# Performance work log

Measured on AMD Instinct MI355X. Metric: run time of the kernel, lower is better.

Reference implementation:

```python
import jax, jax.numpy as jnp
import numpy as np

N_NODES = 100000
N_EDGES = 1600000
N_GRAPHS = 256
IN_F = 64   # global_features (GNN input dim)
OUT_F = 64  # node_features (GNN output dim)


def setup_inputs() -> dict:
    key = jax.random.key(0)
    ks = jax.random.split(key, 8)
    x = jax.random.normal(ks[0], (N_NODES, IN_F), dtype=jnp.float32)
    edge_index = jax.random.randint(ks[1], (2, N_EDGES), 0, N_NODES, dtype=jnp.int64)
    batch = jnp.sort(jax.random.randint(ks[2], (N_NODES,), 0, N_GRAPHS, dtype=jnp.int64))
    # GNNLayer linear: in=global_features, out=node_features
    W_gnn = jax.random.normal(ks[3], (IN_F, OUT_F), dtype=jnp.float32) / np.sqrt(IN_F)
    b_gnn = jnp.zeros((OUT_F,), dtype=jnp.float32)
    # global_attention: Linear(node_features, 1)
    W_att = jax.random.normal(ks[4], (OUT_F, 1), dtype=jnp.float32) / np.sqrt(OUT_F)
    b_att = jnp.zeros((1,), dtype=jnp.float32)
    return {"x": x, "edge_index": edge_index, "batch": batch,
            "W_gnn": W_gnn, "b_gnn": b_gnn, "W_att": W_att, "b_att": b_att}


def reference(x, edge_index, batch, W_gnn, b_gnn, W_att, b_att):
    src, dst = edge_index[0], edge_index[1]
    # --- GNN message passing layer: aggregate neighbor features, transform ---
    agg = jax.ops.segment_sum(x[src], dst, num_segments=N_NODES)  # [N, IN_F]
    h = jax.nn.relu((x + agg) @ W_gnn + b_gnn)                    # [N, OUT_F]
    # --- attention scores + scatter softmax over batch segments ---
    scores = (h @ W_att + b_att)[:, 0]                            # [N]
    seg_max = jax.ops.segment_max(scores, batch, num_segments=N_GRAPHS)
    e = jnp.exp(scores - seg_max[batch])
    denom = jax.ops.segment_sum(e, batch, num_segments=N_GRAPHS)
    w = e / denom[batch]                                          # [N]
    # --- weighted scatter-add pooling ---
    out = jax.ops.segment_sum(w[:, None] * h, batch, num_segments=N_GRAPHS)
    return out  # [N_GRAPHS, OUT_F]
```

## Files before the change

### kernel.cpp

```cpp
#include <hip/hip_runtime.h>

#define N_NODES  100000
#define N_EDGES  1600000
#define N_GRAPHS 256
#define F        64

#define CHUNK    8192
#define NCHUNK   196
#define GBN      128
#define NB2      782
#define EDGE_CAP 2560

#define CAST_ELEMS   (N_NODES * F / 4)
#define CAST_BLOCKS  ((CAST_ELEMS + 1023) / 1024)
#define PREP_BLOCKS  (NCHUNK + CAST_BLOCKS)

__device__ __forceinline__ unsigned short f2bf(float f) {
    unsigned int u = __float_as_uint(f);
    u += 0x7FFFu + ((u >> 16) & 1u);
    return (unsigned short)(u >> 16);
}

__global__ __launch_bounds__(1024) void prep_kernel(
        const float* __restrict__ x, unsigned short* __restrict__ xh,
        const int* __restrict__ src, const int* __restrict__ dst,
        unsigned int* __restrict__ pairs, int* __restrict__ cstartT,
        float* __restrict__ out, float* __restrict__ denom) {
    int tid = threadIdx.x;
    int b   = blockIdx.x;

    if (b >= NCHUNK) {
        int ci = b - NCHUNK;
        if (ci == 0) {
            for (int i = tid; i < N_GRAPHS * F; i += 1024) out[i] = 0.f;
            if (tid < N_GRAPHS) denom[tid] = 0.f;
        }
        int i = ci * 1024 + tid;
        if (i < CAST_ELEMS) {
            float4 v = ((const float4*)x)[i];
            ushort4 o;
            o.x = f2bf(v.x); o.y = f2bf(v.y); o.z = f2bf(v.z); o.w = f2bf(v.w);
            ((ushort4*)xh)[i] = o;
        }
        return;
    }

    __shared__ int hist[NB2];
    __shared__ int cur[NB2];
    __shared__ int wsum[16];
    __shared__ unsigned int stage[CHUNK];
    int c    = b;
    int base = c * CHUNK;
    int m    = min(CHUNK, N_EDGES - base);
    int lane = tid & 63;
    int w    = tid >> 6;

    for (int k = tid; k < NB2; k += 1024) hist[k] = 0;
    __syncthreads();
    for (int e = tid; e < m; e += 1024)
        atomicAdd(&hist[dst[base + e] >> 7], 1);
    __syncthreads();

    int v = (tid < NB2) ? hist[tid] : 0;
    #pragma unroll
    for (int o = 1; o < 64; o <<= 1) {
        int u = __shfl_up(v, o, 64);
        if (lane >= o) v += u;
    }
    if (lane == 63) wsum[w] = v;
    __syncthreads();
    if (tid < 16) {
        int s = wsum[tid];
        #pragma unroll
        for (int o = 1; o < 16; o <<= 1) {
            int u = __shfl_up(s, o, 64);
            if (tid >= o) s += u;
        }
        wsum[tid] = s;
    }
    __syncthreads();
    if (w > 0) v += wsum[w - 1];

    if (tid < NB2) {
        int excl = v - hist[tid];
        cur[tid] = excl;
        cstartT[tid * NCHUNK + c] = base + excl;
    }
    if (tid == 0) cstartT[NB2 * NCHUNK + c] = base + m;
    __syncthreads();
    for (int e = tid; e < m; e += 1024) {
        int d = dst[base + e];
        int slot = atomicAdd(&cur[d >> 7], 1);
        stage[slot] = ((unsigned)(d & (GBN - 1)) << 17) | (unsigned)src[base + e];
    }
    __syncthreads();
    for (int e = tid; e < m; e += 1024)
        pairs[base + e] = stage[e];
}

__global__ __launch_bounds__(512) void compact_kernel(
        const unsigned int* __restrict__ pairs,
        const int* __restrict__ cstartT,
        int* __restrict__ eidx,
        int* __restrict__ nbeg,
        int* __restrict__ nend) {
    __shared__ int rstart[NCHUNK];
    __shared__ int rcnt[NCHUNK];
    __shared__ int roff[NCHUNK];
    __shared__ int wsum[8];
    __shared__ int Etot_s;
    __shared__ unsigned int epairs[EDGE_CAP];
    __shared__ int ncnt[GBN];
    __shared__ int ncur[GBN];

    int tid   = threadIdx.x;
    int wave  = tid >> 6;
    int lane  = tid & 63;
    int b     = blockIdx.x;
    int node0 = b * GBN;
    int nn    = min(GBN, N_NODES - node0);
    int gbase = b * EDGE_CAP;

    int myrc = 0;
    if (tid < NCHUNK) {
        int a = cstartT[b * NCHUNK + tid];
        int n = cstartT[(b + 1) * NCHUNK + tid];
        rstart[tid] = a;
        rcnt[tid]   = n - a;
        myrc = n - a;
    }
    __syncthreads();

    {
        int v = myrc;
        #pragma unroll
        for (int o = 1; o < 64; o <<= 1) {
            int u = __shfl_up(v, o, 64);
            if (lane >= o) v += u;
        }
        if (lane == 63) wsum[wave] = v;
        __syncthreads();
        if (tid < 8) {
            int s = wsum[tid];
            #pragma unroll
            for (int o = 1; o < 8; o <<= 1) {
                int u = __shfl_up(s, o, 64);
                if (tid >= o) s += u;
            }
            wsum[tid] = s;
        }
        __syncthreads();
        if (wave > 0) v += wsum[wave - 1];
        if (tid < NCHUNK) roff[tid] = v - myrc;
        if (tid == NCHUNK - 1) Etot_s = v;
    }
    __syncthreads();
    int E = Etot_s;

    for (int r = wave; r < NCHUNK; r += 8) {
        int cr = rcnt[r];
        for (int l = lane; l < cr; l += 64)
            epairs[roff[r] + l] = pairs[rstart[r] + l];
    }
    __syncthreads();

    if (tid < GBN) ncnt[tid] = 0;
    __syncthreads();
    for (int e = tid; e < E; e += 512)
        atomicAdd(&ncnt[epairs[e] >> 17], 1);
    __syncthreads();
    {
        int mycnt = (tid < GBN) ? ncnt[tid] : 0;
        int v = mycnt;
        #pragma unroll
        for (int o = 1; o < 64; o <<= 1) {
            int u = __shfl_up(v, o, 64);
            if (lane >= o) v += u;
        }
        if (lane == 63) wsum[wave] = v;
        __syncthreads();
        if (tid < 8) {
            int s = wsum[tid];
            #pragma unroll
            for (int o = 1; o < 8; o <<= 1) {
                int u = __shfl_up(s, o, 64);
                if (tid >= o) s += u;
            }
            wsum[tid] = s;
        }
        __syncthreads();
        if (wave > 0) v += wsum[wave - 1];
        if (tid < GBN) {
            int excl = v - mycnt;
            ncur[tid] = excl;
            if (tid < nn) {
                nbeg[node0 + tid] = gbase + excl;
                nend[node0 + tid] = gbase + excl + mycnt;
            }
        }
    }
    __syncthreads();
    for (int e = tid; e < E; e += 512) {
        unsigned int p = epairs[e];
        int slot = atomicAdd(&ncur[p >> 17], 1);
        eidx[gbase + slot] = (int)(p & 0x1FFFFu);
    }
}

#define NODES_PER_WAVE 25
#define GT_NWAVES  (N_NODES / NODES_PER_WAVE)
#define GT_BLOCKS  (GT_NWAVES / 4)

__device__ __forceinline__ float bfl(unsigned int u) { return __uint_as_float(u << 16); }
__device__ __forceinline__ float bfh(unsigned int u) { return __uint_as_float(u & 0xFFFF0000u); }

__global__ __launch_bounds__(256) void gather_pool_kernel(
        const unsigned short* __restrict__ xh,
        const int*   __restrict__ nbeg,
        const int*   __restrict__ nend,
        const int*   __restrict__ eidx,
        const int*   __restrict__ batch,
        const float* __restrict__ Wg,
        const float* __restrict__ bg,
        const float* __restrict__ Wa,
        const float* __restrict__ ba,
        float*       __restrict__ out_acc,
        float*       __restrict__ denom) {
    int tid  = threadIdx.x;
    int lane = tid & 63;
    int grp  = lane >> 3;
    int c    = lane & 7;
    int waveId = blockIdx.x * 4 + (tid >> 6);

    int n0   = waveId * NODES_PER_WAVE;
    int nEnd = n0 + NODES_PER_WAVE;

    float wcol[F];
    #pragma unroll
    for (int k = 0; k < F; ++k) wcol[k] = Wg[k * F + lane];
    float bgl = bg[lane];
    float wal = Wa[lane];
    float ba0 = ba[0];

    const uint4* xh4 = (const uint4*)xh;

    int   cur_g = batch[n0];
    float accw  = 0.f;
    float denw  = 0.f;

    int pb = nbeg[n0];
    int pe = nend[n0];
    int sl_cur = (pb + lane < pe) ? eidx[pb + lane] : 0;

    for (int n = n0; n < nEnd; ++n) {
        int start = pb, end = pe;
        int sl    = sl_cur;
        if (n + 1 < nEnd) {
            pb = nbeg[n + 1];
            pe = nend[n + 1];
            sl_cur = (pb + lane < pe) ? eidx[pb + lane] : 0;
        }

        float a0=0.f,a1=0.f,a2=0.f,a3=0.f,a4=0.f,a5=0.f,a6=0.f,a7=0.f;
        {
            int jmax = end - start; if (jmax > 64) jmax = 64;
            for (int j = 0; j < jmax; j += 8) {
                int el = j + grp;
                int s  = __shfl(sl, el, 64);
                if (el < jmax) {
                    uint4 v = xh4[s * 8 + c];
                    a0 += bfl(v.x); a1 += bfh(v.x);
                    a2 += bfl(v.y); a3 += bfh(v.y);
                    a4 += bfl(v.z); a5 += bfh(v.z);
                    a6 += bfl(v.w); a7 += bfh(v.w);
                }
            }
        }
        for (int base = start + 64; base < end; base += 64) {
            int jmax = end - base; if (jmax > 64) jmax = 64;
            int sl2 = (base + lane < end) ? eidx[base + lane] : 0;
            for (int j = 0; j < jmax; j += 8) {
                int el = j + grp;
                int s  = __shfl(sl2, el, 64);
                if (el < jmax) {
                    uint4 v = xh4[s * 8 + c];
                    a0 += bfl(v.x); a1 += bfh(v.x);
                    a2 += bfl(v.y); a3 += bfh(v.y);
                    a4 += bfl(v.z); a5 += bfh(v.z);
                    a6 += bfl(v.w); a7 += bfh(v.w);
                }
            }
        }
        #pragma unroll
        for (int o = 8; o <= 32; o <<= 1) {
            a0 += __shfl_xor(a0, o, 64); a1 += __shfl_xor(a1, o, 64);
            a2 += __shfl_xor(a2, o, 64); a3 += __shfl_xor(a3, o, 64);
            a4 += __shfl_xor(a4, o, 64); a5 += __shfl_xor(a5, o, 64);
            a6 += __shfl_xor(a6, o, 64); a7 += __shfl_xor(a7, o, 64);
        }
        {
            uint4 v = xh4[n * 8 + c];
            a0 += bfl(v.x); a1 += bfh(v.x);
            a2 += bfl(v.y); a3 += bfh(v.y);
            a4 += bfl(v.z); a5 += bfh(v.z);
            a6 += bfl(v.w); a7 += bfh(v.w);
        }

        float re[8] = {a0,a1,a2,a3,a4,a5,a6,a7};
        float q0=0.f,q1=0.f,q2=0.f,q3=0.f,q4=0.f,q5=0.f,q6=0.f,q7=0.f;
        #pragma unroll
        for (int k = 0; k < F; k += 8) {
            int ln = k >> 3;
            q0 += __int_as_float(__builtin_amdgcn_readlane(__float_as_int(re[0]), ln)) * wcol[k + 0];
            q1 += __int_as_float(__builtin_amdgcn_readlane(__float_as_int(re[1]), ln)) * wcol[k + 1];
            q2 += __int_as_float(__builtin_amdgcn_readlane(__float_as_int(re[2]), ln)) * wcol[k + 2];
            q3 += __int_as_float(__builtin_amdgcn_readlane(__float_as_int(re[3]), ln)) * wcol[k + 3];
            q4 += __int_as_float(__builtin_amdgcn_readlane(__float_as_int(re[4]), ln)) * wcol[k + 4];
            q5 += __int_as_float(__builtin_amdgcn_readlane(__float_as_int(re[5]), ln)) * wcol[k + 5];
            q6 += __int_as_float(__builtin_amdgcn_readlane(__float_as_int(re[6]), ln)) * wcol[k + 6];
            q7 += __int_as_float(__builtin_amdgcn_readlane(__float_as_int(re[7]), ln)) * wcol[k + 7];
        }
        float hv = ((q0 + q1) + (q2 + q3)) + ((q4 + q5) + (q6 + q7)) + bgl;
        hv = hv > 0.f ? hv : 0.f;

        float p = hv * wal;
        #pragma unroll
        for (int o = 32; o > 0; o >>= 1)
            p += __shfl_down(p, o, 64);
        float s = __int_as_float(__builtin_amdgcn_readlane(__float_as_int(p), 0)) + ba0;
        float e = __expf(s);

        int g = batch[n];
        if (g != cur_g) {
            atomicAdd(&out_acc[cur_g * F + lane], accw);
            if (lane == 0) atomicAdd(&denom[cur_g], denw);
            accw = 0.f; denw = 0.f; cur_g = g;
        }
        accw += e * hv;
        denw += e;
    }
    atomicAdd(&out_acc[cur_g * F + lane], accw);
    if (lane == 0) atomicAdd(&denom[cur_g], denw);
}

__global__ __launch_bounds__(256) void finalize_kernel(
        float* __restrict__ out, const float* __restrict__ denom) {
    int i = blockIdx.x * 256 + threadIdx.x;
    if (i >= N_GRAPHS * F) return;
    float d = denom[i >> 6];
    out[i] = (d > 0.f) ? out[i] / d : 0.f;
}

extern "C" void kernel_launch(void* const* d_in, const int* in_sizes, int n_in,
                              void* d_out, int out_size, void* d_ws, size_t ws_size,
                              hipStream_t stream) {
    const float* x     = (const float*)d_in[0];
    const int*   ei    = (const int*)d_in[1];
    const int*   batch = (const int*)d_in[2];
    const float* Wg    = (const float*)d_in[3];
    const float* bg    = (const float*)d_in[4];
    const float* Wa    = (const float*)d_in[5];
    const float* ba    = (const float*)d_in[6];
    float* out = (float*)d_out;

    const int* src = ei;
    const int* dst = ei + N_EDGES;

    char* ws = (char*)d_ws;
    unsigned short* xh      = (unsigned short*)(ws);
    unsigned int*   pairs   = (unsigned int*)(ws + 12800000);
    int*            cstartT = (int*)(ws + 19200000);
    int*            eidx    = (int*)(ws + 19814144);
    int*            nbeg    = (int*)(ws + 27821824);
    int*            nend    = (int*)(ws + 28221824);
    float*          denom   = (float*)(ws + 28621824);

    prep_kernel       <<<PREP_BLOCKS, 1024, 0, stream>>>(
        x, xh, src, dst, pairs, cstartT, out, denom);
    compact_kernel    <<<NB2, 512, 0, stream>>>(pairs, cstartT, eidx, nbeg, nend);
    gather_pool_kernel<<<GT_BLOCKS, 256, 0, stream>>>(
        xh, nbeg, nend, eidx, batch, Wg, bg, Wa, ba, out, denom);
    finalize_kernel   <<<(N_GRAPHS * F + 255) / 256, 256, 0, stream>>>(out, denom);
}
```

Baseline: 189.4 us.

## Move x bf16 cast into compact kernel and flatten segment copy with binary search

The fp32-to-bf16 cast of x and the zeroing of the output now run as extra blocks of the compact kernel instead of the prep kernel, so the prep histogram blocks no longer share a launch with cast work. The compact kernel goes from 512 to 1024 threads. Its per-chunk copy, one wave per segment, is replaced by a flat per-element loop that finds each element's source segment with a binary search over the prefix offsets, which balances load across threads. The cost is extra search work per element and a larger block that may lower occupancy.

```diff
diff --git a/kernel.cpp b/kernel.cpp
--- a/kernel.cpp
+++ b/kernel.cpp
@@ -13,7 +13,7 @@
 
 #define CAST_ELEMS   (N_NODES * F / 4)
 #define CAST_BLOCKS  ((CAST_ELEMS + 1023) / 1024)
-#define PREP_BLOCKS  (NCHUNK + CAST_BLOCKS)
+#define CPF_BLOCKS   (NB2 + CAST_BLOCKS)
 
 __device__ __forceinline__ unsigned short f2bf(float f) {
     unsigned int u = __float_as_uint(f);
@@ -22,15 +22,76 @@
 }
 
 __global__ __launch_bounds__(1024) void prep_kernel(
-        const float* __restrict__ x, unsigned short* __restrict__ xh,
         const int* __restrict__ src, const int* __restrict__ dst,
-        unsigned int* __restrict__ pairs, int* __restrict__ cstartT,
+        unsigned int* __restrict__ pairs, int* __restrict__ cstartT) {
+    __shared__ int hist[NB2];
+    __shared__ int cur[NB2];
+    __shared__ int wsum[16];
+    __shared__ unsigned int stage[CHUNK];
+    int tid  = threadIdx.x;
+    int c    = blockIdx.x;
+    int base = c * CHUNK;
+    int m    = min(CHUNK, N_EDGES - base);
+    int lane = tid & 63;
+    int w    = tid >> 6;
+
+    for (int k = tid; k < NB2; k += 1024) hist[k] = 0;
+    __syncthreads();
+    for (int e = tid; e < m; e += 1024)
+        atomicAdd(&hist[dst[base + e] >> 7], 1);
+    __syncthreads();
+
+    int v = (tid < NB2) ? hist[tid] : 0;
+    #pragma unroll
+    for (int o = 1; o < 64; o <<= 1) {
+        int u = __shfl_up(v, o, 64);
+        if (lane >= o) v += u;
+    }
+    if (lane == 63) wsum[w] = v;
+    __syncthreads();
+    if (tid < 16) {
+        int s = wsum[tid];
+        #pragma unroll
+        for (int o = 1; o < 16; o <<= 1) {
+            int u = __shfl_up(s, o, 64);
+            if (tid >= o) s += u;
+        }
+        wsum[tid] = s;
+    }
+    __syncthreads();
+    if (w > 0) v += wsum[w - 1];
+
+    if (tid < NB2) {
+        int excl = v - hist[tid];
+        cur[tid] = excl;
+        cstartT[tid * NCHUNK + c] = base + excl;
+    }
+    if (tid == 0) cstartT[NB2 * NCHUNK + c] = base + m;
+    __syncthreads();
+    for (int e = tid; e < m; e += 1024) {
+        int d = dst[base + e];
+        int slot = atomicAdd(&cur[d >> 7], 1);
+        stage[slot] = ((unsigned)(d & (GBN - 1)) << 17) | (unsigned)src[base + e];
+    }
+    __syncthreads();
+    for (int e = tid; e < m; e += 1024)
+        pairs[base + e] = stage[e];
+}
+
+__global__ __launch_bounds__(1024) void compact_cast_kernel(
+        const unsigned int* __restrict__ pairs,
+        const int* __restrict__ cstartT,
+        int* __restrict__ eidx,
+        int* __restrict__ nbeg,
+        int* __restrict__ nend,
+        const float* __restrict__ x,
+        unsigned short* __restrict__ xh,
         float* __restrict__ out, float* __restrict__ denom) {
     int tid = threadIdx.x;
     int b   = blockIdx.x;
 
-    if (b >= NCHUNK) {
-        int ci = b - NCHUNK;
+    if (b >= NB2) {
+        int ci = b - NB2;
         if (ci == 0) {
             for (int i = tid; i < N_GRAPHS * F; i += 1024) out[i] = 0.f;
             if (tid < N_GRAPHS) denom[tid] = 0.f;
@@ -45,78 +106,15 @@
         return;
     }
 
-    __shared__ int hist[NB2];
-    __shared__ int cur[NB2];
+    __shared__ int rstart[NCHUNK];
+    __shared__ int roff[NCHUNK + 1];
     __shared__ int wsum[16];
-    __shared__ unsigned int stage[CHUNK];
-    int c    = b;
-    int base = c * CHUNK;
-    int m    = min(CHUNK, N_EDGES - base);
-    int lane = tid & 63;
-    int w    = tid >> 6;
-
-    for (int k = tid; k < NB2; k += 1024) hist[k] = 0;
-    __syncthreads();
-    for (int e = tid; e < m; e += 1024)
-        atomicAdd(&hist[dst[base + e] >> 7], 1);
-    __syncthreads();
-
-    int v = (tid < NB2) ? hist[tid] : 0;
-    #pragma unroll
-    for (int o = 1; o < 64; o <<= 1) {
-        int u = __shfl_up(v, o, 64);
-        if (lane >= o) v += u;
-    }
-    if (lane == 63) wsum[w] = v;
-    __syncthreads();
-    if (tid < 16) {
-        int s = wsum[tid];
-        #pragma unroll
-        for (int o = 1; o < 16; o <<= 1) {
-            int u = __shfl_up(s, o, 64);
-            if (tid >= o) s += u;
-        }
-        wsum[tid] = s;
-    }
-    __syncthreads();
-    if (w > 0) v += wsum[w - 1];
-
-    if (tid < NB2) {
-        int excl = v - hist[tid];
-        cur[tid] = excl;
-        cstartT[tid * NCHUNK + c] = base + excl;
-    }
-    if (tid == 0) cstartT[NB2 * NCHUNK + c] = base + m;
-    __syncthreads();
-    for (int e = tid; e < m; e += 1024) {
-        int d = dst[base + e];
-        int slot = atomicAdd(&cur[d >> 7], 1);
-        stage[slot] = ((unsigned)(d & (GBN - 1)) << 17) | (unsigned)src[base + e];
-    }
-    __syncthreads();
-    for (int e = tid; e < m; e += 1024)
-        pairs[base + e] = stage[e];
-}
-
-__global__ __launch_bounds__(512) void compact_kernel(
-        const unsigned int* __restrict__ pairs,
-        const int* __restrict__ cstartT,
-        int* __restrict__ eidx,
-        int* __restrict__ nbeg,
-        int* __restrict__ nend) {
-    __shared__ int rstart[NCHUNK];
-    __shared__ int rcnt[NCHUNK];
-    __shared__ int roff[NCHUNK];
-    __shared__ int wsum[8];
-    __shared__ int Etot_s;
     __shared__ unsigned int epairs[EDGE_CAP];
     __shared__ int ncnt[GBN];
     __shared__ int ncur[GBN];
 
-    int tid   = threadIdx.x;
     int wave  = tid >> 6;
     int lane  = tid & 63;
-    int b     = blockIdx.x;
     int node0 = b * GBN;
     int nn    = min(GBN, N_NODES - node0);
     int gbase = b * EDGE_CAP;
@@ -126,7 +124,6 @@
         int a = cstartT[b * NCHUNK + tid];
         int n = cstartT[(b + 1) * NCHUNK + tid];
         rstart[tid] = a;
-        rcnt[tid]   = n - a;
         myrc = n - a;
     }
     __syncthreads();
@@ -140,10 +137,10 @@
         }
         if (lane == 63) wsum[wave] = v;
         __syncthreads();
-        if (tid < 8) {
+        if (tid < 16) {
             int s = wsum[tid];
             #pragma unroll
-            for (int o = 1; o < 8; o <<= 1) {
+            for (int o = 1; o < 16; o <<= 1) {
                 int u = __shfl_up(s, o, 64);
                 if (tid >= o) s += u;
             }
@@ -152,21 +149,24 @@
         __syncthreads();
         if (wave > 0) v += wsum[wave - 1];
         if (tid < NCHUNK) roff[tid] = v - myrc;
-        if (tid == NCHUNK - 1) Etot_s = v;
-    }
-    __syncthreads();
-    int E = Etot_s;
-
-    for (int r = wave; r < NCHUNK; r += 8) {
-        int cr = rcnt[r];
-        for (int l = lane; l < cr; l += 64)
-            epairs[roff[r] + l] = pairs[rstart[r] + l];
+        if (tid == NCHUNK - 1) roff[NCHUNK] = v;
+    }
+    __syncthreads();
+    int E = roff[NCHUNK];
+
+    for (int e = tid; e < E; e += 1024) {
+        int lo = 0, hi = NCHUNK - 1;
+        while (lo < hi) {
+            int mid = (lo + hi + 1) >> 1;
+            if (roff[mid] <= e) lo = mid; else hi = mid - 1;
+        }
+        epairs[e] = pairs[rstart[lo] + (e - roff[lo])];
     }
     __syncthreads();
 
     if (tid < GBN) ncnt[tid] = 0;
     __syncthreads();
-    for (int e = tid; e < E; e += 512)
+    for (int e = tid; e < E; e += 1024)
         atomicAdd(&ncnt[epairs[e] >> 17], 1);
     __syncthreads();
     {
@@ -179,17 +179,14 @@
         }
         if (lane == 63) wsum[wave] = v;
         __syncthreads();
-        if (tid < 8) {
+        if (tid < 2) {
             int s = wsum[tid];
-            #pragma unroll
-            for (int o = 1; o < 8; o <<= 1) {
-                int u = __shfl_up(s, o, 64);
-                if (tid >= o) s += u;
-            }
+            int u = __shfl_up(s, 1, 64);
+            if (tid >= 1) s += u;
             wsum[tid] = s;
         }
         __syncthreads();
-        if (wave > 0) v += wsum[wave - 1];
+        if (wave == 1) v += wsum[0];
         if (tid < GBN) {
             int excl = v - mycnt;
             ncur[tid] = excl;
@@ -200,7 +197,7 @@
         }
     }
     __syncthreads();
-    for (int e = tid; e < E; e += 512) {
+    for (int e = tid; e < E; e += 1024) {
         unsigned int p = epairs[e];
         int slot = atomicAdd(&ncur[p >> 17], 1);
         eidx[gbase + slot] = (int)(p & 0x1FFFFu);
@@ -375,10 +372,10 @@
     int*            nend    = (int*)(ws + 28221824);
     float*          denom   = (float*)(ws + 28621824);
 
-    prep_kernel       <<<PREP_BLOCKS, 1024, 0, stream>>>(
-        x, xh, src, dst, pairs, cstartT, out, denom);
-    compact_kernel    <<<NB2, 512, 0, stream>>>(pairs, cstartT, eidx, nbeg, nend);
-    gather_pool_kernel<<<GT_BLOCKS, 256, 0, stream>>>(
+    prep_kernel        <<<NCHUNK, 1024, 0, stream>>>(src, dst, pairs, cstartT);
+    compact_cast_kernel<<<CPF_BLOCKS, 1024, 0, stream>>>(
+        pairs, cstartT, eidx, nbeg, nend, x, xh, out, denom);
+    gather_pool_kernel <<<GT_BLOCKS, 256, 0, stream>>>(
         xh, nbeg, nend, eidx, batch, Wg, bg, Wa, ba, out, denom);
-    finalize_kernel   <<<(N_GRAPHS * F + 255) / 256, 256, 0, stream>>>(out, denom);
-}
+    finalize_kernel    <<<(N_GRAPHS * F + 255) / 256, 256, 0, stream>>>(out, denom);
+}
```

Result: faster. 184.5 us (-2.6%).
